# Kernel tuning notes

Hardware: AMD Instinct MI355X
Metric: run time of the kernel (lower is better)

The kernel has to match this reference:

```python
import jax, jax.numpy as jnp
import numpy as np

B, H, S, D = 1, 16, 4096, 64
TEMPERATURE = 8.0          # sqrt(d_k)
WINDOW_SIZE = 256
HALF_WINDOW = WINDOW_SIZE // 2
NEG_INF = -1000000000.0


def setup_inputs() -> dict:
    key = jax.random.key(0)
    kq, kk, kv = jax.random.split(key, 3)
    q = jax.random.normal(kq, (B, H, S, D), dtype=jnp.float32)
    k = jax.random.normal(kk, (B, H, S, D), dtype=jnp.float32)
    v = jax.random.normal(kv, (B, H, S, D), dtype=jnp.float32)
    return {"q": q, "k": k, "v": v}


def reference(q, k, v):
    # q,k,v: [B,H,S,D]
    seq = q.shape[2]
    attn = jnp.einsum('bhqd,bhkd->bhqk', q, k) / TEMPERATURE  # [B,H,S,S]
    if seq > WINDOW_SIZE:
        idx = jnp.arange(seq)
        # torch loop: row i allows columns [i-half, i+half] inclusive
        win = jnp.abs(idx[:, None] - idx[None, :]) <= HALF_WINDOW  # [S,S]
        attn = jnp.where(win[None, None, :, :], attn, NEG_INF)
    attn = jax.nn.softmax(attn, axis=-1)  # dropout p=0 -> identity
    out = jnp.einsum('bhqk,bhkd->bhqd', attn, v)
    return (out, attn)
```

## Files before the change

### kernel.cpp

```cpp
#include <hip/hip_runtime.h>
#include <hip/hip_bf16.h>


typedef short bf16x8 __attribute__((ext_vector_type(8)));
typedef float f32x4  __attribute__((ext_vector_type(4)));
typedef unsigned int u32;
typedef unsigned short u16;

namespace {
constexpr int S = 4096, H = 16, Dh = 64, TR = 16, HW = 128, NCH = 5;
constexpr int UW  = NCH * 64;
constexpr int KP  = 72;
constexpr int PBW = UW + 8;
}

__device__ __forceinline__ u16 f2bf(float x) {
    u32 u = __float_as_uint(x);
    return (u16)((u + 0x7fffu + ((u >> 16) & 1u)) >> 16);
}
__device__ __forceinline__ float bf2f(u16 h) {
    return __uint_as_float(((u32)h) << 16);
}

__device__ __forceinline__ void bar_lds() {
    asm volatile("s_waitcnt lgkmcnt(0)" ::: "memory");
    __builtin_amdgcn_s_barrier();
    asm volatile("" ::: "memory");
}

__global__ __launch_bounds__(256, 4)
void wattn(const float* __restrict__ q, const float* __restrict__ k,
           const float* __restrict__ v, float* __restrict__ out,
           float* __restrict__ attn)
{
    __shared__ __align__(16) u16 hbuf[16768];
    __shared__ float red[TR * 4];
    __shared__ float inv_row[TR];
    u16* qh_ = hbuf;
    u16* ql_ = hbuf + 1152;
    u16* kh_ = hbuf + 2304;
    u16* kl_ = hbuf + 6912;
    u16* pb_ = hbuf + 11520;

    const int tid  = threadIdx.x;
    const int wave = tid >> 6, lane = tid & 63;
    const int g = lane >> 4, m = lane & 15;

    int bx = blockIdx.x;
    bx = (bx & 7) * (H * (S / TR) / 8) + (bx >> 3);
    const int h  = bx >> 8;
    const int r0 = (bx & 255) * TR;
    const int c0 = max(0, r0 - HW);
    const int c1 = min(S - 1, r0 + TR - 1 + HW);
    const int c0q = c0 >> 2;

    const float* qp = q + ((size_t)h * S + r0) * Dh;
    const float* kp = k + (size_t)h * S * Dh;
    const float* vp = v + (size_t)h * S * Dh;
    float* arow = attn + ((size_t)h * S + r0) * S;

    {
        const int row = tid >> 4, d4 = (tid & 15) * 4;
        float4 t = *(const float4*)(qp + row * Dh + d4);
        float xs[4] = {t.x, t.y, t.z, t.w};
        u16* dh = qh_ + row * KP + d4;
        u16* dl = ql_ + row * KP + d4;
        #pragma unroll
        for (int i = 0; i < 4; ++i) {
            u16 hi = f2bf(xs[i]);
            dh[i] = hi;
            dl[i] = f2bf(xs[i] - bf2f(hi));
        }
    }
    bar_lds();

    bf16x8 aqh[2], aql[2];
    #pragma unroll
    for (int ks = 0; ks < 2; ++ks) {
        aqh[ks] = *(const bf16x8*)(qh_ + m * KP + ks * 32 + g * 8);
        aql[ks] = *(const bf16x8*)(ql_ + m * KP + ks * 32 + g * 8);
    }

    f32x4 sc[NCH];
    #pragma unroll
    for (int cc = 0; cc < NCH; ++cc) {
        {
            const int col = tid >> 2, d16 = (tid & 3) * 16;
            const int cg  = min(c0 + cc * 64 + col, S - 1);
            const float* src = kp + (size_t)cg * Dh + d16;
            u16* dh = kh_ + col * KP + d16;
            u16* dl = kl_ + col * KP + d16;
            #pragma unroll
            for (int i4 = 0; i4 < 4; ++i4) {
                float4 t = *(const float4*)(src + i4 * 4);
                float xs[4] = {t.x, t.y, t.z, t.w};
                #pragma unroll
                for (int i = 0; i < 4; ++i) {
                    u16 hi = f2bf(xs[i]);
                    dh[i4 * 4 + i] = hi;
                    dl[i4 * 4 + i] = f2bf(xs[i] - bf2f(hi));
                }
            }
        }
        {
            const float4 z4 = {0.f, 0.f, 0.f, 0.f};
            const int rbeg = cc * 3;
            const int rend = (cc == NCH - 1) ? TR : rbeg + 3;
            for (int r = rbeg; r < rend; ++r) {
                float4* dst = (float4*)(arow + (size_t)r * S);
                #pragma unroll
                for (int kk4 = 0; kk4 < 4; ++kk4) {
                    const int c4 = tid + 256 * kk4;
                    if ((unsigned)(c4 - c0q) >= (unsigned)(UW / 4)) dst[c4] = z4;
                }
            }
        }
        bar_lds();
        f32x4 acc = {0.f, 0.f, 0.f, 0.f};
        #pragma unroll
        for (int ks = 0; ks < 2; ++ks) {
            bf16x8 bh = *(const bf16x8*)(kh_ + (wave * 16 + m) * KP + ks * 32 + g * 8);
            bf16x8 bl = *(const bf16x8*)(kl_ + (wave * 16 + m) * KP + ks * 32 + g * 8);
            acc = __builtin_amdgcn_mfma_f32_16x16x32_bf16(aqh[ks], bh, acc, 0, 0, 0);
            acc = __builtin_amdgcn_mfma_f32_16x16x32_bf16(aql[ks], bh, acc, 0, 0, 0);
            acc = __builtin_amdgcn_mfma_f32_16x16x32_bf16(aqh[ks], bl, acc, 0, 0, 0);
        }
        sc[cc] = acc;
        bar_lds();
    }

    float rs[4] = {0.f, 0.f, 0.f, 0.f};
    #pragma unroll
    for (int cc = 0; cc < NCH; ++cc) {
        const int colg = c0 + cc * 64 + wave * 16 + m;
        #pragma unroll
        for (int w = 0; w < 4; ++w) {
            const int row = r0 + g * 4 + w;
            const float l = sc[cc][w] * 0.125f;
            const bool ok = (colg >= row - HW) && (colg <= row + HW) && (colg <= c1);
            const float ev = ok ? __expf(l) : 0.f;
            rs[w] += ev;
            pb_[(g * 4 + w) * PBW + cc * 64 + wave * 16 + m] = f2bf(ev);
        }
    }
    #pragma unroll
    for (int off = 1; off < 16; off <<= 1) {
        #pragma unroll
        for (int w = 0; w < 4; ++w) rs[w] += __shfl_xor(rs[w], off, 64);
    }
    if (m == 0) {
        #pragma unroll
        for (int w = 0; w < 4; ++w) red[(g * 4 + w) * 4 + wave] = rs[w];
    }
    bar_lds();
    if (tid < TR) {
        float4 p4 = *(const float4*)(red + tid * 4);
        inv_row[tid] = 1.0f / (p4.x + p4.y + p4.z + p4.w);
    }
    bar_lds();

    {
        #pragma unroll
        for (int ii = 0; ii < 5; ++ii) {
            const int i = tid + 256 * ii;
            const int r = i / (UW / 4);
            const int c = i - r * (UW / 4);
            const int c4 = c0q + c;
            if (c4 < S / 4) {
                ushort4 hh = *(const ushort4*)(pb_ + r * PBW + c * 4);
                const float inv = inv_row[r];
                float4 val;
                val.x = bf2f(hh.x) * inv; val.y = bf2f(hh.y) * inv;
                val.z = bf2f(hh.z) * inv; val.w = bf2f(hh.w) * inv;
                ((float4*)(arow + (size_t)r * S))[c4] = val;
            }
        }
    }

    f32x4 oacc = {0.f, 0.f, 0.f, 0.f};
    for (int cc = 0; cc < NCH; ++cc) {
        bar_lds();
        const int j = tid & 63, dbase = (tid >> 6) * 16;
        const int jg = min(c0 + cc * 64 + j, S - 1);
        const float* src = vp + (size_t)jg * Dh + dbase;
        #pragma unroll
        for (int i4 = 0; i4 < 4; ++i4) {
            float4 t = *(const float4*)(src + i4 * 4);
            float xs[4] = {t.x, t.y, t.z, t.w};
            #pragma unroll
            for (int i = 0; i < 4; ++i)
                kh_[(dbase + i4 * 4 + i) * KP + j] = f2bf(xs[i]);
        }
        bar_lds();
        #pragma unroll
        for (int ks = 0; ks < 2; ++ks) {
            bf16x8 ap = *(const bf16x8*)(pb_ + m * PBW + cc * 64 + ks * 32 + g * 8);
            bf16x8 bv = *(const bf16x8*)(kh_ + (wave * 16 + m) * KP + ks * 32 + g * 8);
            oacc = __builtin_amdgcn_mfma_f32_16x16x32_bf16(ap, bv, oacc, 0, 0, 0);
        }
    }

    float4 inv4 = *(const float4*)(inv_row + g * 4);
    float* op = out + (((size_t)h * S + r0 + g * 4) * Dh) + wave * 16 + m;
    #pragma unroll
    for (int w = 0; w < 4; ++w) {
        const float iw = (w == 0) ? inv4.x : (w == 1) ? inv4.y : (w == 2) ? inv4.z : inv4.w;
        op[(size_t)w * Dh] = oacc[w] * iw;
    }
}

extern "C" void kernel_launch(void* const* d_in, const int* in_sizes, int n_in,
                              void* d_out, int out_size, void* d_ws, size_t ws_size,
                              hipStream_t stream) {
    const float* q = (const float*)d_in[0];
    const float* k = (const float*)d_in[1];
    const float* v = (const float*)d_in[2];
    float* out  = (float*)d_out;
    float* attn = out + (size_t)H * S * Dh;
    wattn<<<dim3(H * (S / TR)), dim3(256), 0, stream>>>(q, k, v, out, attn);
}
```

Baseline: 1.113 ms.

## Double-buffer K/V tiles with register prefetch and unify attn row writes

Loads Q directly into MFMA registers instead of staging it through LDS. K and V chunks are now prefetched into registers one step ahead and written into double-buffered LDS, which removes one barrier per chunk. The zero-fill of the attention matrix and the probability writeback are merged into one final pass that writes every row coalesced. The larger LDS footprint lowers the occupancy target from 4 to 3 blocks per CU. All attention-matrix stores now sit at the end of the kernel instead of overlapping with compute, which risks exposing the store traffic.

```diff
diff --git a/kernel.cpp b/kernel.cpp
--- a/kernel.cpp
+++ b/kernel.cpp
@@ -12,6 +12,8 @@
 constexpr int UW  = NCH * 64;
 constexpr int KP  = 72;
 constexpr int PBW = UW + 8;
+constexpr int NTILE = H * (S / TR);
+constexpr int KBUF = 2 * 64 * KP;
 }
 
 __device__ __forceinline__ u16 f2bf(float x) {
@@ -28,26 +30,22 @@
     asm volatile("" ::: "memory");
 }
 
-__global__ __launch_bounds__(256, 4)
+__global__ __launch_bounds__(256, 3)
 void wattn(const float* __restrict__ q, const float* __restrict__ k,
            const float* __restrict__ v, float* __restrict__ out,
            float* __restrict__ attn)
 {
-    __shared__ __align__(16) u16 hbuf[16768];
+    __shared__ __align__(16) u16 hbuf[2 * KBUF + TR * PBW];
     __shared__ float red[TR * 4];
     __shared__ float inv_row[TR];
-    u16* qh_ = hbuf;
-    u16* ql_ = hbuf + 1152;
-    u16* kh_ = hbuf + 2304;
-    u16* kl_ = hbuf + 6912;
-    u16* pb_ = hbuf + 11520;
+    u16* pb_ = hbuf + 2 * KBUF;
 
     const int tid  = threadIdx.x;
     const int wave = tid >> 6, lane = tid & 63;
     const int g = lane >> 4, m = lane & 15;
 
     int bx = blockIdx.x;
-    bx = (bx & 7) * (H * (S / TR) / 8) + (bx >> 3);
+    bx = (bx & 7) * (NTILE / 8) + (bx >> 3);
     const int h  = bx >> 8;
     const int r0 = (bx & 255) * TR;
     const int c0 = max(0, r0 - HW);
@@ -59,41 +57,39 @@
     const float* vp = v + (size_t)h * S * Dh;
     float* arow = attn + ((size_t)h * S + r0) * S;
 
-    {
-        const int row = tid >> 4, d4 = (tid & 15) * 4;
-        float4 t = *(const float4*)(qp + row * Dh + d4);
-        float xs[4] = {t.x, t.y, t.z, t.w};
-        u16* dh = qh_ + row * KP + d4;
-        u16* dl = ql_ + row * KP + d4;
-        #pragma unroll
-        for (int i = 0; i < 4; ++i) {
+    bf16x8 aqh[2], aql[2];
+    #pragma unroll
+    for (int ks = 0; ks < 2; ++ks) {
+        const float* qsrc = qp + m * Dh + ks * 32 + g * 8;
+        float4 t0 = *(const float4*)(qsrc);
+        float4 t1 = *(const float4*)(qsrc + 4);
+        float xs[8] = {t0.x, t0.y, t0.z, t0.w, t1.x, t1.y, t1.z, t1.w};
+        #pragma unroll
+        for (int i = 0; i < 8; ++i) {
             u16 hi = f2bf(xs[i]);
-            dh[i] = hi;
-            dl[i] = f2bf(xs[i] - bf2f(hi));
-        }
-    }
-    bar_lds();
-
-    bf16x8 aqh[2], aql[2];
-    #pragma unroll
-    for (int ks = 0; ks < 2; ++ks) {
-        aqh[ks] = *(const bf16x8*)(qh_ + m * KP + ks * 32 + g * 8);
-        aql[ks] = *(const bf16x8*)(ql_ + m * KP + ks * 32 + g * 8);
-    }
-
+            aqh[ks][i] = (short)hi;
+            aql[ks][i] = (short)f2bf(xs[i] - bf2f(hi));
+        }
+    }
+
+    const int col = tid >> 2, d16 = (tid & 3) * 16;
+    float4 rk[4];
+    {
+        const float* src = kp + (size_t)min(c0 + col, S - 1) * Dh + d16;
+        #pragma unroll
+        for (int i4 = 0; i4 < 4; ++i4) rk[i4] = *(const float4*)(src + i4 * 4);
+    }
     f32x4 sc[NCH];
     #pragma unroll
     for (int cc = 0; cc < NCH; ++cc) {
+        u16* kh = hbuf + (cc & 1) * KBUF;
+        u16* kl = kh + 64 * KP;
         {
-            const int col = tid >> 2, d16 = (tid & 3) * 16;
-            const int cg  = min(c0 + cc * 64 + col, S - 1);
-            const float* src = kp + (size_t)cg * Dh + d16;
-            u16* dh = kh_ + col * KP + d16;
-            u16* dl = kl_ + col * KP + d16;
+            u16* dh = kh + col * KP + d16;
+            u16* dl = kl + col * KP + d16;
             #pragma unroll
             for (int i4 = 0; i4 < 4; ++i4) {
-                float4 t = *(const float4*)(src + i4 * 4);
-                float xs[4] = {t.x, t.y, t.z, t.w};
+                float xs[4] = {rk[i4].x, rk[i4].y, rk[i4].z, rk[i4].w};
                 #pragma unroll
                 for (int i = 0; i < 4; ++i) {
                     u16 hi = f2bf(xs[i]);
@@ -102,31 +98,31 @@
                 }
             }
         }
-        {
-            const float4 z4 = {0.f, 0.f, 0.f, 0.f};
-            const int rbeg = cc * 3;
-            const int rend = (cc == NCH - 1) ? TR : rbeg + 3;
-            for (int r = rbeg; r < rend; ++r) {
-                float4* dst = (float4*)(arow + (size_t)r * S);
-                #pragma unroll
-                for (int kk4 = 0; kk4 < 4; ++kk4) {
-                    const int c4 = tid + 256 * kk4;
-                    if ((unsigned)(c4 - c0q) >= (unsigned)(UW / 4)) dst[c4] = z4;
-                }
-            }
+        if (cc + 1 < NCH) {
+            const float* src =
+                kp + (size_t)min(c0 + (cc + 1) * 64 + col, S - 1) * Dh + d16;
+            #pragma unroll
+            for (int i4 = 0; i4 < 4; ++i4) rk[i4] = *(const float4*)(src + i4 * 4);
         }
         bar_lds();
         f32x4 acc = {0.f, 0.f, 0.f, 0.f};
         #pragma unroll
         for (int ks = 0; ks < 2; ++ks) {
-            bf16x8 bh = *(const bf16x8*)(kh_ + (wave * 16 + m) * KP + ks * 32 + g * 8);
-            bf16x8 bl = *(const bf16x8*)(kl_ + (wave * 16 + m) * KP + ks * 32 + g * 8);
+            bf16x8 bh = *(const bf16x8*)(kh + (wave * 16 + m) * KP + ks * 32 + g * 8);
+            bf16x8 bl = *(const bf16x8*)(kl + (wave * 16 + m) * KP + ks * 32 + g * 8);
             acc = __builtin_amdgcn_mfma_f32_16x16x32_bf16(aqh[ks], bh, acc, 0, 0, 0);
             acc = __builtin_amdgcn_mfma_f32_16x16x32_bf16(aql[ks], bh, acc, 0, 0, 0);
             acc = __builtin_amdgcn_mfma_f32_16x16x32_bf16(aqh[ks], bl, acc, 0, 0, 0);
         }
         sc[cc] = acc;
-        bar_lds();
+    }
+
+    const int j = tid & 63, dbase = (tid >> 6) * 16;
+    float4 rv[4];
+    {
+        const float* src = vp + (size_t)min(c0 + j, S - 1) * Dh + dbase;
+        #pragma unroll
+        for (int i4 = 0; i4 < 4; ++i4) rv[i4] = *(const float4*)(src + i4 * 4);
     }
 
     float rs[4] = {0.f, 0.f, 0.f, 0.f};
@@ -159,53 +155,58 @@
     }
     bar_lds();
 
-    {
-        #pragma unroll
-        for (int ii = 0; ii < 5; ++ii) {
-            const int i = tid + 256 * ii;
-            const int r = i / (UW / 4);
-            const int c = i - r * (UW / 4);
-            const int c4 = c0q + c;
-            if (c4 < S / 4) {
-                ushort4 hh = *(const ushort4*)(pb_ + r * PBW + c * 4);
-                const float inv = inv_row[r];
-                float4 val;
-                val.x = bf2f(hh.x) * inv; val.y = bf2f(hh.y) * inv;
-                val.z = bf2f(hh.z) * inv; val.w = bf2f(hh.w) * inv;
-                ((float4*)(arow + (size_t)r * S))[c4] = val;
-            }
-        }
-    }
-
     f32x4 oacc = {0.f, 0.f, 0.f, 0.f};
+    #pragma unroll
     for (int cc = 0; cc < NCH; ++cc) {
-        bar_lds();
-        const int j = tid & 63, dbase = (tid >> 6) * 16;
-        const int jg = min(c0 + cc * 64 + j, S - 1);
-        const float* src = vp + (size_t)jg * Dh + dbase;
+        u16* vt = hbuf + (cc & 1) * KBUF;
         #pragma unroll
         for (int i4 = 0; i4 < 4; ++i4) {
-            float4 t = *(const float4*)(src + i4 * 4);
-            float xs[4] = {t.x, t.y, t.z, t.w};
+            float xs[4] = {rv[i4].x, rv[i4].y, rv[i4].z, rv[i4].w};
             #pragma unroll
             for (int i = 0; i < 4; ++i)
-                kh_[(dbase + i4 * 4 + i) * KP + j] = f2bf(xs[i]);
+                vt[(dbase + i4 * 4 + i) * KP + j] = f2bf(xs[i]);
+        }
+        if (cc + 1 < NCH) {
+            const float* src = vp + (size_t)min(c0 + (cc + 1) * 64 + j, S - 1) * Dh + dbase;
+            #pragma unroll
+            for (int i4 = 0; i4 < 4; ++i4) rv[i4] = *(const float4*)(src + i4 * 4);
         }
         bar_lds();
         #pragma unroll
         for (int ks = 0; ks < 2; ++ks) {
             bf16x8 ap = *(const bf16x8*)(pb_ + m * PBW + cc * 64 + ks * 32 + g * 8);
-            bf16x8 bv = *(const bf16x8*)(kh_ + (wave * 16 + m) * KP + ks * 32 + g * 8);
+            bf16x8 bv = *(const bf16x8*)(vt + (wave * 16 + m) * KP + ks * 32 + g * 8);
             oacc = __builtin_amdgcn_mfma_f32_16x16x32_bf16(ap, bv, oacc, 0, 0, 0);
         }
     }
 
-    float4 inv4 = *(const float4*)(inv_row + g * 4);
-    float* op = out + (((size_t)h * S + r0 + g * 4) * Dh) + wave * 16 + m;
-    #pragma unroll
-    for (int w = 0; w < 4; ++w) {
-        const float iw = (w == 0) ? inv4.x : (w == 1) ? inv4.y : (w == 2) ? inv4.z : inv4.w;
-        op[(size_t)w * Dh] = oacc[w] * iw;
+    {
+        float4 inv4 = *(const float4*)(inv_row + g * 4);
+        float* op = out + (((size_t)h * S + r0 + g * 4) * Dh) + wave * 16 + m;
+        #pragma unroll
+        for (int w = 0; w < 4; ++w) {
+            const float iw = (w == 0) ? inv4.x : (w == 1) ? inv4.y : (w == 2) ? inv4.z : inv4.w;
+            op[(size_t)w * Dh] = oacc[w] * iw;
+        }
+    }
+
+    {
+        for (int r = 0; r < TR; ++r) {
+            const float inv = inv_row[r];
+            float4* dst = (float4*)(arow + (size_t)r * S);
+            #pragma unroll
+            for (int kk4 = 0; kk4 < 4; ++kk4) {
+                const int c4 = tid + 256 * kk4;
+                const int o4 = c4 - c0q;
+                float4 val = {0.f, 0.f, 0.f, 0.f};
+                if ((unsigned)o4 < (unsigned)(UW / 4)) {
+                    ushort4 hh = *(const ushort4*)(pb_ + r * PBW + o4 * 4);
+                    val.x = bf2f(hh.x) * inv; val.y = bf2f(hh.y) * inv;
+                    val.z = bf2f(hh.z) * inv; val.w = bf2f(hh.w) * inv;
+                }
+                dst[c4] = val;
+            }
+        }
     }
 }
 
@@ -217,5 +218,5 @@
     const float* v = (const float*)d_in[2];
     float* out  = (float*)d_out;
     float* attn = out + (size_t)H * S * Dh;
-    wattn<<<dim3(H * (S / TR)), dim3(256), 0, stream>>>(q, k, v, out, attn);
-}
+    wattn<<<dim3(NTILE), dim3(256), 0, stream>>>(q, k, v, out, attn);
+}
```

New measurement: 1.093 ms. About the same (-1.8%).
